# Optimization experiments

Measured on AMD Instinct MI355X. Metric: run time of the kernel, lower is better.

Reference implementation:

```python
import jax, jax.numpy as jnp
import numpy as np

D_IN = 256
DIMS = 256


def setup_inputs() -> dict:
    key = jax.random.key(0)
    k1, k2, k3, k4, k5 = jax.random.split(key, 5)
    B, Tq, Tk = 4, 512, 512
    query = jax.random.normal(k1, (B, Tq, D_IN), dtype=jnp.float32)
    value = jax.random.normal(k2, (B, Tk, D_IN), dtype=jnp.float32)
    # Dense(dims, use_bias=False) kernels (glorot-like scale) and AdditiveAttention scale vector
    Wq = jax.random.normal(k3, (D_IN, DIMS), dtype=jnp.float32) / np.sqrt(D_IN)
    Wv = jax.random.normal(k4, (D_IN, DIMS), dtype=jnp.float32) / np.sqrt(D_IN)
    scale = jax.random.normal(k5, (DIMS,), dtype=jnp.float32)
    return {"query": query, "value": value, "Wq": Wq, "Wv": Wv, "scale": scale}


def reference(query, value, Wq, Wv, scale):
    # q_proj: [B,Tq,d], k_proj: [B,Tk,d]; attention value = RAW value tensor (as in source)
    q = jnp.einsum("bqi,id->bqd", query, Wq)
    k = jnp.einsum("bki,id->bkd", value, Wv)
    # Additive (Bahdanau) scores: [B,Tq,Tk] via broadcast tanh then reduce with scale
    scores = jnp.einsum("bqkd,d->bqk", jnp.tanh(q[:, :, None, :] + k[:, None, :, :]), scale)
    attn = jax.nn.softmax(scores, axis=-1)  # masks are all-ones -> no-op
    out = jnp.einsum("bqk,bki->bqi", attn, value)
    return out, attn
```

## Files before the change

kernel.cpp:

```cpp
#include <hip/hip_runtime.h>

#define LOG2E 1.4426950408889634f
#define TWO_LOG2E 2.885390081777927f

__device__ __forceinline__ float fast_exp2(float x) { return __builtin_amdgcn_exp2f(x); }
__device__ __forceinline__ float fast_rcp(float x)  { return __builtin_amdgcn_rcpf(x); }

__global__ __launch_bounds__(256) void proj_kernel(
    const float* __restrict__ query, const float* __restrict__ value,
    const float* __restrict__ Wq, const float* __restrict__ Wv,
    float* __restrict__ eq, float* __restrict__ ek)
{
    __shared__ float in_lds[8 * 256];
    const int t = threadIdx.x;
    const int row0 = blockIdx.x * 8;
    const float* src; const float* W; float* dst;
    if (row0 < 2048) { src = query + (size_t)row0 * 256; W = Wq; dst = eq + (size_t)row0 * 256; }
    else { const int r = row0 - 2048; src = value + (size_t)r * 256; W = Wv; dst = ek + (size_t)r * 256; }

    const float4* s4 = (const float4*)src;
    float4* l4 = (float4*)in_lds;
    l4[t] = s4[t];
    l4[t + 256] = s4[t + 256];
    __syncthreads();

    float acc[8];
#pragma unroll
    for (int r = 0; r < 8; ++r) acc[r] = 0.f;

    for (int d = 0; d < 256; d += 4) {
        const float w0 = W[(d + 0) * 256 + t];
        const float w1 = W[(d + 1) * 256 + t];
        const float w2 = W[(d + 2) * 256 + t];
        const float w3 = W[(d + 3) * 256 + t];
#pragma unroll
        for (int r = 0; r < 8; ++r) {
            const float4 v = *(const float4*)&in_lds[r * 256 + d];
            acc[r] = fmaf(v.x, w0, acc[r]);
            acc[r] = fmaf(v.y, w1, acc[r]);
            acc[r] = fmaf(v.z, w2, acc[r]);
            acc[r] = fmaf(v.w, w3, acc[r]);
        }
    }
#pragma unroll
    for (int r = 0; r < 8; ++r) dst[r * 256 + t] = fast_exp2(acc[r] * TWO_LOG2E);
}

#define SQ_STRIDE 66
__global__ __launch_bounds__(256) void scores_kernel(
    const float* __restrict__ eq, const float* __restrict__ ek,
    const float* __restrict__ scale, float* __restrict__ attn)
{
    __shared__ float q_lds[32 * SQ_STRIDE];
    __shared__ float k_lds[32 * SQ_STRIDE];
    __shared__ float sc_lds[256];

    const int t = threadIdx.x;
    const int tx = t & 15, ty = t >> 4;
    const int b = blockIdx.z, qt = blockIdx.y, kt = blockIdx.x;
    const float* qbase = eq + (size_t)(b * 512 + qt * 32) * 256;
    const float* kbase = ek + (size_t)(b * 512 + kt * 32) * 256;

    sc_lds[t] = -2.f * scale[t];

    float a00 = 0.f, a01 = 0.f, a10 = 0.f, a11 = 0.f;

    for (int dc = 0; dc < 256; dc += 64) {
        __syncthreads();
#pragma unroll
        for (int l = 0; l < 2; ++l) {
            const int f = t + 256 * l;
            const int row = f >> 4, c4 = (f & 15) * 4;
            const float4 qv = *(const float4*)&qbase[row * 256 + dc + c4];
            const float4 kv = *(const float4*)&kbase[row * 256 + dc + c4];
            *(float2*)&q_lds[row * SQ_STRIDE + c4]     = make_float2(qv.x, qv.y);
            *(float2*)&q_lds[row * SQ_STRIDE + c4 + 2] = make_float2(qv.z, qv.w);
            *(float2*)&k_lds[row * SQ_STRIDE + c4]     = make_float2(kv.x, kv.y);
            *(float2*)&k_lds[row * SQ_STRIDE + c4 + 2] = make_float2(kv.z, kv.w);
        }
        __syncthreads();

#pragma unroll 4
        for (int d = 0; d < 64; d += 2) {
            const float2 s2 = *(const float2*)&sc_lds[dc + d];
            const float2 qa = *(const float2*)&q_lds[(ty * 2 + 0) * SQ_STRIDE + d];
            const float2 qb = *(const float2*)&q_lds[(ty * 2 + 1) * SQ_STRIDE + d];
            const float2 ka = *(const float2*)&k_lds[(tx * 2 + 0) * SQ_STRIDE + d];
            const float2 kb = *(const float2*)&k_lds[(tx * 2 + 1) * SQ_STRIDE + d];

            a00 = fmaf(s2.x, fast_rcp(fmaf(qa.x, ka.x, 1.f)), a00);
            a01 = fmaf(s2.x, fast_rcp(fmaf(qa.x, kb.x, 1.f)), a01);
            a10 = fmaf(s2.x, fast_rcp(fmaf(qb.x, ka.x, 1.f)), a10);
            a11 = fmaf(s2.x, fast_rcp(fmaf(qb.x, kb.x, 1.f)), a11);
            a00 = fmaf(s2.y, fast_rcp(fmaf(qa.y, ka.y, 1.f)), a00);
            a01 = fmaf(s2.y, fast_rcp(fmaf(qa.y, kb.y, 1.f)), a01);
            a10 = fmaf(s2.y, fast_rcp(fmaf(qb.y, ka.y, 1.f)), a10);
            a11 = fmaf(s2.y, fast_rcp(fmaf(qb.y, kb.y, 1.f)), a11);
        }
    }

    const int qrow = qt * 32 + ty * 2;
    const int kcol = kt * 32 + tx * 2;
    *(float2*)&attn[(size_t)(b * 512 + qrow + 0) * 512 + kcol] = make_float2(a00, a01);
    *(float2*)&attn[(size_t)(b * 512 + qrow + 1) * 512 + kcol] = make_float2(a10, a11);
}

__global__ __launch_bounds__(64) void softmax_kernel(float* __restrict__ attn)
{
    const int row = blockIdx.x;
    float4* p4 = (float4*)(attn + (size_t)row * 512);
    const int t = threadIdx.x;
    float4 a = p4[t];
    float4 b = p4[t + 64];

    float m = fmaxf(fmaxf(fmaxf(a.x, a.y), fmaxf(a.z, a.w)),
                    fmaxf(fmaxf(b.x, b.y), fmaxf(b.z, b.w)));
#pragma unroll
    for (int off = 32; off; off >>= 1) m = fmaxf(m, __shfl_xor(m, off));

    a.x = fast_exp2((a.x - m) * LOG2E); a.y = fast_exp2((a.y - m) * LOG2E);
    a.z = fast_exp2((a.z - m) * LOG2E); a.w = fast_exp2((a.w - m) * LOG2E);
    b.x = fast_exp2((b.x - m) * LOG2E); b.y = fast_exp2((b.y - m) * LOG2E);
    b.z = fast_exp2((b.z - m) * LOG2E); b.w = fast_exp2((b.w - m) * LOG2E);

    float sum = ((a.x + a.y) + (a.z + a.w)) + ((b.x + b.y) + (b.z + b.w));
#pragma unroll
    for (int off = 32; off; off >>= 1) sum += __shfl_xor(sum, off);

    const float inv = fast_rcp(sum);
    a.x *= inv; a.y *= inv; a.z *= inv; a.w *= inv;
    b.x *= inv; b.y *= inv; b.z *= inv; b.w *= inv;
    p4[t] = a; p4[t + 64] = b;
}

#define AT_ST 68
#define VT_ST 68
__global__ __launch_bounds__(256) void pv_kernel(
    const float* __restrict__ attn, const float* __restrict__ value,
    float* __restrict__ out)
{
    __shared__ float a_lds[32 * AT_ST];
    __shared__ float v_lds[64 * VT_ST];

    const int t = threadIdx.x;
    const int tx = t & 15, ty = t >> 4;
    const int b = blockIdx.z, qt = blockIdx.y, it = blockIdx.x;
    const int q0 = qt * 32, i0 = it * 64;
    const float* abase = attn + (size_t)(b * 512 + q0) * 512;
    const float* vbase = value + (size_t)(b * 512) * 256 + i0;

    float4 acc0 = {0, 0, 0, 0}, acc1 = {0, 0, 0, 0};

    for (int kc = 0; kc < 512; kc += 64) {
        __syncthreads();
#pragma unroll
        for (int l = 0; l < 2; ++l) {
            const int f = t + 256 * l;
            const int row = f >> 4, c4 = (f & 15) * 4;
            *(float4*)&a_lds[row * AT_ST + c4] = *(const float4*)&abase[row * 512 + kc + c4];
        }
#pragma unroll
        for (int l = 0; l < 4; ++l) {
            const int f = t + 256 * l;
            const int row = f >> 4, c4 = (f & 15) * 4;
            *(float4*)&v_lds[row * VT_ST + c4] = *(const float4*)&vbase[(size_t)(kc + row) * 256 + c4];
        }
        __syncthreads();

        for (int k = 0; k < 64; ++k) {
            const float a0 = a_lds[(ty * 2 + 0) * AT_ST + k];
            const float a1 = a_lds[(ty * 2 + 1) * AT_ST + k];
            const float4 v = *(const float4*)&v_lds[k * VT_ST + tx * 4];
            acc0.x = fmaf(a0, v.x, acc0.x); acc0.y = fmaf(a0, v.y, acc0.y);
            acc0.z = fmaf(a0, v.z, acc0.z); acc0.w = fmaf(a0, v.w, acc0.w);
            acc1.x = fmaf(a1, v.x, acc1.x); acc1.y = fmaf(a1, v.y, acc1.y);
            acc1.z = fmaf(a1, v.z, acc1.z); acc1.w = fmaf(a1, v.w, acc1.w);
        }
    }

    float* obase = out + (size_t)(b * 512 + q0) * 256 + i0;
    *(float4*)&obase[(ty * 2 + 0) * 256 + tx * 4] = acc0;
    *(float4*)&obase[(ty * 2 + 1) * 256 + tx * 4] = acc1;
}

extern "C" void kernel_launch(void* const* d_in, const int* in_sizes, int n_in,
                              void* d_out, int out_size, void* d_ws, size_t ws_size,
                              hipStream_t stream) {
    const float* query = (const float*)d_in[0];
    const float* value = (const float*)d_in[1];
    const float* Wq    = (const float*)d_in[2];
    const float* Wv    = (const float*)d_in[3];
    const float* scale = (const float*)d_in[4];

    float* out0 = (float*)d_out;
    float* attn = out0 + 4 * 512 * 256;

    float* eq = (float*)d_ws;
    float* ek = eq + 2048 * 256;

    proj_kernel<<<512, 256, 0, stream>>>(query, value, Wq, Wv, eq, ek);
    scores_kernel<<<dim3(16, 16, 4), 256, 0, stream>>>(eq, ek, scale, attn);
    softmax_kernel<<<2048, 64, 0, stream>>>(attn);
    pv_kernel<<<dim3(4, 16, 4), 256, 0, stream>>>(attn, value, out0);
}
```

Measured before the change: 72.79 us.

## Split scores over feature halves and pair reciprocals to halve rcp count

```diff
diff --git a/kernel.cpp b/kernel.cpp
--- a/kernel.cpp
+++ b/kernel.cpp
@@ -46,72 +46,88 @@
     for (int r = 0; r < 8; ++r) dst[r * 256 + t] = fast_exp2(acc[r] * TWO_LOG2E);
 }
 
-#define SQ_STRIDE 66
+#define SQ_ST 130
 __global__ __launch_bounds__(256) void scores_kernel(
     const float* __restrict__ eq, const float* __restrict__ ek,
-    const float* __restrict__ scale, float* __restrict__ attn)
-{
-    __shared__ float q_lds[32 * SQ_STRIDE];
-    __shared__ float k_lds[32 * SQ_STRIDE];
-    __shared__ float sc_lds[256];
+    const float* __restrict__ scale,
+    float* __restrict__ part0, float* __restrict__ part1)
+{
+    __shared__ float q_lds[32 * SQ_ST];
+    __shared__ float k_lds[32 * SQ_ST];
+    __shared__ float sc_lds[128];
 
     const int t = threadIdx.x;
     const int tx = t & 15, ty = t >> 4;
-    const int b = blockIdx.z, qt = blockIdx.y, kt = blockIdx.x;
-    const float* qbase = eq + (size_t)(b * 512 + qt * 32) * 256;
-    const float* kbase = ek + (size_t)(b * 512 + kt * 32) * 256;
-
-    sc_lds[t] = -2.f * scale[t];
+    const int kt = blockIdx.x, qt = blockIdx.y;
+    const int b = blockIdx.z >> 1, dh = blockIdx.z & 1;
+    const int d0 = dh * 128;
+    const float* qbase = eq + (size_t)(b * 512 + qt * 32) * 256 + d0;
+    const float* kbase = ek + (size_t)(b * 512 + kt * 32) * 256 + d0;
+
+    if (t < 128) sc_lds[t] = -2.f * scale[d0 + t];
+
+#pragma unroll
+    for (int l = 0; l < 4; ++l) {
+        const int idx = t + 256 * l;
+        const int row = idx >> 5, c4 = (idx & 31) * 4;
+        const float4 qv = *(const float4*)&qbase[row * 256 + c4];
+        const float4 kv = *(const float4*)&kbase[row * 256 + c4];
+        *(float2*)&q_lds[row * SQ_ST + c4]     = make_float2(qv.x, qv.y);
+        *(float2*)&q_lds[row * SQ_ST + c4 + 2] = make_float2(qv.z, qv.w);
+        *(float2*)&k_lds[row * SQ_ST + c4]     = make_float2(kv.x, kv.y);
+        *(float2*)&k_lds[row * SQ_ST + c4 + 2] = make_float2(kv.z, kv.w);
+    }
+    __syncthreads();
 
     float a00 = 0.f, a01 = 0.f, a10 = 0.f, a11 = 0.f;
 
-    for (int dc = 0; dc < 256; dc += 64) {
-        __syncthreads();
-#pragma unroll
-        for (int l = 0; l < 2; ++l) {
-            const int f = t + 256 * l;
-            const int row = f >> 4, c4 = (f & 15) * 4;
-            const float4 qv = *(const float4*)&qbase[row * 256 + dc + c4];
-            const float4 kv = *(const float4*)&kbase[row * 256 + dc + c4];
-            *(float2*)&q_lds[row * SQ_STRIDE + c4]     = make_float2(qv.x, qv.y);
-            *(float2*)&q_lds[row * SQ_STRIDE + c4 + 2] = make_float2(qv.z, qv.w);
-            *(float2*)&k_lds[row * SQ_STRIDE + c4]     = make_float2(kv.x, kv.y);
-            *(float2*)&k_lds[row * SQ_STRIDE + c4 + 2] = make_float2(kv.z, kv.w);
-        }
-        __syncthreads();
-
 #pragma unroll 4
-        for (int d = 0; d < 64; d += 2) {
-            const float2 s2 = *(const float2*)&sc_lds[dc + d];
-            const float2 qa = *(const float2*)&q_lds[(ty * 2 + 0) * SQ_STRIDE + d];
-            const float2 qb = *(const float2*)&q_lds[(ty * 2 + 1) * SQ_STRIDE + d];
-            const float2 ka = *(const float2*)&k_lds[(tx * 2 + 0) * SQ_STRIDE + d];
-            const float2 kb = *(const float2*)&k_lds[(tx * 2 + 1) * SQ_STRIDE + d];
-
-            a00 = fmaf(s2.x, fast_rcp(fmaf(qa.x, ka.x, 1.f)), a00);
-            a01 = fmaf(s2.x, fast_rcp(fmaf(qa.x, kb.x, 1.f)), a01);
-            a10 = fmaf(s2.x, fast_rcp(fmaf(qb.x, ka.x, 1.f)), a10);
-            a11 = fmaf(s2.x, fast_rcp(fmaf(qb.x, kb.x, 1.f)), a11);
-            a00 = fmaf(s2.y, fast_rcp(fmaf(qa.y, ka.y, 1.f)), a00);
-            a01 = fmaf(s2.y, fast_rcp(fmaf(qa.y, kb.y, 1.f)), a01);
-            a10 = fmaf(s2.y, fast_rcp(fmaf(qb.y, ka.y, 1.f)), a10);
-            a11 = fmaf(s2.y, fast_rcp(fmaf(qb.y, kb.y, 1.f)), a11);
-        }
-    }
-
+    for (int d = 0; d < 128; d += 2) {
+        const float2 s2 = *(const float2*)&sc_lds[d];
+        const float2 qa = *(const float2*)&q_lds[(ty * 2 + 0) * SQ_ST + d];
+        const float2 qb = *(const float2*)&q_lds[(ty * 2 + 1) * SQ_ST + d];
+        const float2 ka = *(const float2*)&k_lds[(tx * 2 + 0) * SQ_ST + d];
+        const float2 kb = *(const float2*)&k_lds[(tx * 2 + 1) * SQ_ST + d];
+
+        {
+            const float A = fmaf(qa.x, ka.x, 1.f), B = fmaf(qa.y, ka.y, 1.f);
+            a00 = fmaf(fmaf(s2.y, A, s2.x * B), fast_rcp(A * B), a00);
+        }
+        {
+            const float A = fmaf(qa.x, kb.x, 1.f), B = fmaf(qa.y, kb.y, 1.f);
+            a01 = fmaf(fmaf(s2.y, A, s2.x * B), fast_rcp(A * B), a01);
+        }
+        {
+            const float A = fmaf(qb.x, ka.x, 1.f), B = fmaf(qb.y, ka.y, 1.f);
+            a10 = fmaf(fmaf(s2.y, A, s2.x * B), fast_rcp(A * B), a10);
+        }
+        {
+            const float A = fmaf(qb.x, kb.x, 1.f), B = fmaf(qb.y, kb.y, 1.f);
+            a11 = fmaf(fmaf(s2.y, A, s2.x * B), fast_rcp(A * B), a11);
+        }
+    }
+
+    float* part = dh ? part1 : part0;
     const int qrow = qt * 32 + ty * 2;
     const int kcol = kt * 32 + tx * 2;
-    *(float2*)&attn[(size_t)(b * 512 + qrow + 0) * 512 + kcol] = make_float2(a00, a01);
-    *(float2*)&attn[(size_t)(b * 512 + qrow + 1) * 512 + kcol] = make_float2(a10, a11);
-}
-
-__global__ __launch_bounds__(64) void softmax_kernel(float* __restrict__ attn)
+    *(float2*)&part[(size_t)(b * 512 + qrow + 0) * 512 + kcol] = make_float2(a00, a01);
+    *(float2*)&part[(size_t)(b * 512 + qrow + 1) * 512 + kcol] = make_float2(a10, a11);
+}
+
+__global__ __launch_bounds__(64) void softmax_kernel(
+    const float* __restrict__ part0, const float* __restrict__ part1,
+    float* __restrict__ attn)
 {
     const int row = blockIdx.x;
-    float4* p4 = (float4*)(attn + (size_t)row * 512);
-    const int t = threadIdx.x;
-    float4 a = p4[t];
-    float4 b = p4[t + 64];
+    const float4* p0 = (const float4*)(part0 + (size_t)row * 512);
+    const float4* p1 = (const float4*)(part1 + (size_t)row * 512);
+    float4* po = (float4*)(attn + (size_t)row * 512);
+    const int t = threadIdx.x;
+
+    float4 a = p0[t], a2 = p1[t];
+    a.x += a2.x; a.y += a2.y; a.z += a2.z; a.w += a2.w;
+    float4 b = p0[t + 64], b2 = p1[t + 64];
+    b.x += b2.x; b.y += b2.y; b.z += b2.z; b.w += b2.w;
 
     float m = fmaxf(fmaxf(fmaxf(a.x, a.y), fmaxf(a.z, a.w)),
                     fmaxf(fmaxf(b.x, b.y), fmaxf(b.z, b.w)));
@@ -130,7 +146,7 @@
     const float inv = fast_rcp(sum);
     a.x *= inv; a.y *= inv; a.z *= inv; a.w *= inv;
     b.x *= inv; b.y *= inv; b.z *= inv; b.w *= inv;
-    p4[t] = a; p4[t + 64] = b;
+    po[t] = a; po[t + 64] = b;
 }
 
 #define AT_ST 68
@@ -195,11 +211,13 @@
     float* out0 = (float*)d_out;
     float* attn = out0 + 4 * 512 * 256;
 
-    float* eq = (float*)d_ws;
-    float* ek = eq + 2048 * 256;
+    float* eq    = (float*)d_ws;
+    float* ek    = eq + 2048 * 256;
+    float* part0 = ek + 2048 * 256;
+    float* part1 = part0 + 4 * 512 * 512;
 
     proj_kernel<<<512, 256, 0, stream>>>(query, value, Wq, Wv, eq, ek);
-    scores_kernel<<<dim3(16, 16, 4), 256, 0, stream>>>(eq, ek, scale, attn);
-    softmax_kernel<<<2048, 64, 0, stream>>>(attn);
+    scores_kernel<<<dim3(16, 16, 8), 256, 0, stream>>>(eq, ek, scale, part0, part1);
+    softmax_kernel<<<2048, 64, 0, stream>>>(part0, part1, attn);
     pv_kernel<<<dim3(4, 16, 4), 256, 0, stream>>>(attn, value, out0);
 }
```

Measured after the change: 73.11 us. No clear change (+0.4%).
